# Kernel optimization log

Measured on AMD Instinct MI355X. Metric: run time of the kernel, lower is better.

## Reference

```python
import jax, jax.numpy as jnp
import numpy as np

NEG_SLOPE = 0.2  # PyG GATConv default leaky_relu slope


def gat_layer(x, W, a_src, a_dst, b):
    # x: [B, N, Fin]; W: [Fin, H*C]; a_src/a_dst: [H, C]; b: [H*C]
    # Dense-block equivalent of PyG GATConv on a fully-connected block graph
    # (self loops included), concat=True.
    B, N, Fin = x.shape
    H, C = a_src.shape
    h = jnp.einsum('bnf,fhc->bnhc', x, W.reshape(Fin, H, C))  # [B,N,H,C]
    ls = jnp.einsum('bnhc,hc->bnh', h, a_src)  # alpha_src per node
    ld = jnp.einsum('bnhc,hc->bnh', h, a_dst)  # alpha_dst per node
    # logits[i, j] = leaky_relu(alpha_dst[i] + alpha_src[j]); softmax over j
    logits = jax.nn.leaky_relu(ld[:, :, None, :] + ls[:, None, :, :], NEG_SLOPE)  # [B,i,j,H]
    attn = jax.nn.softmax(logits, axis=2)
    out = jnp.einsum('bijh,bjhc->bihc', attn, h).reshape(B, N, H * C)
    return out + b


def setup_inputs() -> dict:
    key = jax.random.key(0)
    ks = jax.random.split(key, 12)
    bs, R, Nc, enc = 8, 256, 64, 31
    H, hid, out = 8, 64, 32
    Fin = 1 + enc  # 32
    p = lambda k, shape: jax.random.normal(k, shape, jnp.float32) * 0.05
    return {
        'xs': jax.random.normal(ks[0], (bs, R, Nc), jnp.float32),
        'pos_enc': jax.random.normal(ks[1], (bs, Nc, enc), jnp.float32),
        'W1': p(ks[2], (Fin, H * hid)), 'as1': p(ks[3], (H, hid)), 'ad1': p(ks[4], (H, hid)),
        'b1': jnp.zeros((H * hid,), jnp.float32),
        'W2': p(ks[5], (H * hid, H * hid)), 'as2': p(ks[6], (H, hid)), 'ad2': p(ks[7], (H, hid)),
        'b2': jnp.zeros((H * hid,), jnp.float32),
        'W3': p(ks[8], (H * hid, H * out)), 'as3': p(ks[9], (H, out)), 'ad3': p(ks[10], (H, out)),
        'b3': jnp.zeros((H * out,), jnp.float32),
    }


def reference(xs, pos_enc, W1, as1, ad1, b1, W2, as2, ad2, b2, W3, as3, ad3, b3):
    bs, R, Nc = xs.shape
    enc = pos_enc.shape[-1]
    pe = jnp.broadcast_to(pos_enc[:, None], (bs, R, Nc, enc))
    x = jnp.concatenate([xs[..., None], pe], axis=-1)  # [bs,R,Nc,1+enc]
    x = x.reshape(bs * R, Nc, 1 + enc)  # independent fully-connected blocks
    x = gat_layer(x, W1, as1, ad1, b1)
    x = gat_layer(x, W2, as2, ad2, b2)
    x = gat_layer(x, W3, as3, ad3, b3)
    out = x.reshape(bs, R, Nc, -1).mean(axis=2)  # mean over num_xs
    return out
```

## Files before the change

### kernel.cpp

```cpp
#include <hip/hip_runtime.h>
#include <hip/hip_bf16.h>

typedef __hip_bfloat16 bf16;
typedef unsigned int uint32;
typedef __attribute__((ext_vector_type(8))) short short8;
typedef __attribute__((ext_vector_type(4))) float float4v;

#define THREADS 512
#define LDX 520
#define LDE 68

__device__ __forceinline__ bf16 f2b(float x) { return __float2bfloat16(x); }
__device__ __forceinline__ uint32 packbf2(float x, float y) {
  union { __hip_bfloat162 b; uint32 u; } cv;
  cv.b = __float22bfloat162_rn(make_float2(x, y));
  return cv.u;
}

__global__ void convw_all(const float* __restrict__ W1,
                          const float* __restrict__ W2,
                          const float* __restrict__ W3, bf16* __restrict__ dst) {
  int o = blockIdx.x * 256 + threadIdx.x;
  if (o >= 409600) return;
  const float* W;
  int Mlog, loc;
  if (o < 16384) { W = W1; Mlog = 9; loc = o; }
  else if (o < 278528) { W = W2; Mlog = 9; loc = o - 16384; }
  else { W = W3; Mlog = 8; loc = o - 278528; }
  int j = loc & 7, kc = (loc >> 3) & 3, rest = loc >> 5;
  int M = 1 << Mlog;
  int n = rest & (M - 1), kb = rest >> Mlog;
  int k = kb * 32 + kc * 8 + j;
  dst[o] = f2b(W[(size_t)k * M + n]);
}

__global__ void convE_all(
    const float* __restrict__ W1, const float* __restrict__ as1, const float* __restrict__ ad1,
    const float* __restrict__ W2, const float* __restrict__ as2, const float* __restrict__ ad2,
    const float* __restrict__ W3, const float* __restrict__ as3, const float* __restrict__ ad3,
    bf16* __restrict__ dstE) {
  int o = blockIdx.x * 256 + threadIdx.x;
  if (o >= 16896) return;
  const float *W, *as_, *ad_;
  int M, C, loc;
  if (o < 512) { loc = o; W = W1; as_ = as1; ad_ = ad1; M = 512; C = 64; }
  else if (o < 8704) { loc = o - 512; W = W2; as_ = as2; ad_ = ad2; M = 512; C = 64; }
  else { loc = o - 8704; W = W3; as_ = as3; ad_ = ad3; M = 256; C = 32; }
  int j = loc & 7, kc = (loc >> 3) & 3, n = (loc >> 5) & 15, ks = loc >> 9;
  int k = ks * 32 + kc * 8 + j;
  int head = n & 7;
  const float* a = (n < 8) ? as_ : ad_;
  float s = 0.f;
  for (int c = 0; c < C; ++c)
    s += W[(size_t)k * M + head * C + c] * a[head * C + c];
  dstE[o] = f2b(s);
}

template <int K, int M, int C, bool LAST>
__device__ __forceinline__ void gat_layer(
    int t, const bf16* __restrict__ Wswz, const bf16* __restrict__ WE,
    const float* __restrict__ bias, bf16* sX, float* sE) {
  constexpr int CT = M / 128;
  constexpr int CTO = CT / 2;
  constexpr int KS = K / 32;
  const int lane = t & 63;
  const int hu = __builtin_amdgcn_readfirstlane(t >> 6);
  const int ln = lane & 15;
  const int kq = lane >> 4;
  const int colbase = hu * (M / 8);

  const bf16* aptr = sX + ln * LDX + kq * 8;
  const bf16* aptrE = sX + (hu * 16 + ln) * LDX + kq * 8;
  const bf16* eptr = WE + ln * 32 + kq * 8;

  uint32 Ppk[CT][4][2];

#pragma unroll
  for (int cto = 0; cto < CTO; ++cto) {
    float4v acc[4][2];
    float4v acce = (float4v)0.f;
#pragma unroll
    for (int rt = 0; rt < 4; ++rt) {
      acc[rt][0] = (float4v)0.f;
      acc[rt][1] = (float4v)0.f;
    }
    const bf16* bptr = Wswz + (colbase + cto * 32 + ln) * 32 + kq * 8;
    if (cto == 0 && hu < 4) {
#pragma unroll 4
      for (int ks = 0; ks < KS; ++ks) {
        short8 afr[4];
#pragma unroll
        for (int rt = 0; rt < 4; ++rt)
          afr[rt] = *(const short8*)(aptr + rt * 16 * LDX + ks * 32);
        short8 bfr[2];
        bfr[0] = *(const short8*)(bptr + (size_t)ks * (M * 32));
        bfr[1] = *(const short8*)(bptr + (size_t)ks * (M * 32) + 16 * 32);
        short8 efr = *(const short8*)(eptr + ks * 512);
        short8 afrE = *(const short8*)(aptrE + ks * 32);
        acce = __builtin_amdgcn_mfma_f32_16x16x32_bf16(afrE, efr, acce, 0, 0, 0);
#pragma unroll
        for (int rt = 0; rt < 4; ++rt) {
          acc[rt][0] = __builtin_amdgcn_mfma_f32_16x16x32_bf16(
              afr[rt], bfr[0], acc[rt][0], 0, 0, 0);
          acc[rt][1] = __builtin_amdgcn_mfma_f32_16x16x32_bf16(
              afr[rt], bfr[1], acc[rt][1], 0, 0, 0);
        }
      }
      *(float4v*)(sE + ln * LDE + hu * 16 + kq * 4) = acce;
    } else {
#pragma unroll 4
      for (int ks = 0; ks < KS; ++ks) {
        short8 afr[4];
#pragma unroll
        for (int rt = 0; rt < 4; ++rt)
          afr[rt] = *(const short8*)(aptr + rt * 16 * LDX + ks * 32);
        short8 bfr[2];
        bfr[0] = *(const short8*)(bptr + (size_t)ks * (M * 32));
        bfr[1] = *(const short8*)(bptr + (size_t)ks * (M * 32) + 16 * 32);
#pragma unroll
        for (int rt = 0; rt < 4; ++rt) {
          acc[rt][0] = __builtin_amdgcn_mfma_f32_16x16x32_bf16(
              afr[rt], bfr[0], acc[rt][0], 0, 0, 0);
          acc[rt][1] = __builtin_amdgcn_mfma_f32_16x16x32_bf16(
              afr[rt], bfr[1], acc[rt][1], 0, 0, 0);
        }
      }
    }
#pragma unroll
    for (int ci = 0; ci < 2; ++ci)
#pragma unroll
      for (int rt = 0; rt < 4; ++rt) {
        Ppk[cto * 2 + ci][rt][0] = packbf2(acc[rt][ci][0], acc[rt][ci][1]);
        Ppk[cto * 2 + ci][rt][1] = packbf2(acc[rt][ci][2], acc[rt][ci][3]);
      }
  }

  __syncthreads();

  const float* lsrow = sE + hu * LDE;
  const float* ldrow = sE + (8 + hu) * LDE;
  float lsj[2][8];
#pragma unroll
  for (int s = 0; s < 2; ++s) {
    float4 v0 = *(const float4*)(lsrow + s * 32 + kq * 8);
    float4 v1 = *(const float4*)(lsrow + s * 32 + kq * 8 + 4);
    lsj[s][0] = v0.x; lsj[s][1] = v0.y; lsj[s][2] = v0.z; lsj[s][3] = v0.w;
    lsj[s][4] = v1.x; lsj[s][5] = v1.y; lsj[s][6] = v1.z; lsj[s][7] = v1.w;
  }
  short8 pfr[4][2];
#pragma unroll
  for (int rt = 0; rt < 4; ++rt) {
    const float ldi = ldrow[rt * 16 + ln];
    float pe_[2][8];
    float rsum = 0.f;
#pragma unroll
    for (int s = 0; s < 2; ++s)
#pragma unroll
      for (int jj = 0; jj < 8; ++jj) {
        float tt = ldi + lsj[s][jj];
        float l = fmaxf(tt, 0.2f * tt);
        float e = __expf(l);
        pe_[s][jj] = e;
        rsum += e;
      }
    rsum += __shfl_xor(rsum, 16, 64);
    rsum += __shfl_xor(rsum, 32, 64);
    const float ri = 1.0f / rsum;
#pragma unroll
    for (int s = 0; s < 2; ++s) {
      union { uint32 q[4]; short8 s8; } w;
#pragma unroll
      for (int jp = 0; jp < 4; ++jp)
        w.q[jp] = packbf2(pe_[s][2 * jp] * ri, pe_[s][2 * jp + 1] * ri);
      pfr[rt][s] = w.s8;
    }
  }

  const int kqhi = kq >> 1;
  const int addrA = 4 * (ln + 16 * ((kq & 1) << 1));
#pragma unroll
  for (int ct = 0; ct < CT; ++ct) {
    short8 hfr[2];
#pragma unroll
    for (int s = 0; s < 2; ++s) {
      union { uint32 q[4]; short8 s8; } u;
#pragma unroll
      for (int jjp = 0; jjp < 4; ++jjp) {
        int addr = addrA + ((jjp >> 1) << 6);
        int lo = __builtin_amdgcn_ds_bpermute(addr, (int)Ppk[ct][2 * s + 0][jjp & 1]);
        int hi = __builtin_amdgcn_ds_bpermute(addr, (int)Ppk[ct][2 * s + 1][jjp & 1]);
        u.q[jjp] = kqhi ? (uint32)hi : (uint32)lo;
      }
      hfr[s] = u.s8;
    }
    float4v oacc[4];
#pragma unroll
    for (int rt = 0; rt < 4; ++rt) oacc[rt] = (float4v)0.f;
#pragma unroll
    for (int s = 0; s < 2; ++s)
#pragma unroll
      for (int rt = 0; rt < 4; ++rt)
        oacc[rt] = __builtin_amdgcn_mfma_f32_16x16x32_bf16(
            pfr[rt][s], hfr[s], oacc[rt], 0, 0, 0);
    const float bv = bias[colbase + ct * 16 + ln];
#pragma unroll
    for (int rt = 0; rt < 4; ++rt)
#pragma unroll
      for (int r = 0; r < 4; ++r) {
        float val = oacc[rt][r] + bv;
        int row = rt * 16 + kq * 4 + r;
        if constexpr (LAST)
          ((float*)sX)[row * 260 + colbase + ct * 16 + ln] = val;
        else
          sX[row * LDX + colbase + ct * 16 + ln] = f2b(val);
      }
  }
  __syncthreads();
}

__global__ __launch_bounds__(THREADS, 4) void gat3_mfma(
    const float* __restrict__ xs, const float* __restrict__ pe,
    const bf16* __restrict__ W1s, const bf16* __restrict__ WE1,
    const float* __restrict__ b1, const bf16* __restrict__ W2s,
    const bf16* __restrict__ WE2, const float* __restrict__ b2,
    const bf16* __restrict__ W3s, const bf16* __restrict__ WE3,
    const float* __restrict__ b3, float* __restrict__ out) {
  extern __shared__ char smem[];
  bf16* sX = (bf16*)smem;
  float* sE = (float*)(smem + 66560);

  const int t = threadIdx.x;
  const int blk = blockIdx.x;
  const int bidx = blk >> 8;

  for (int idx = t; idx < 64 * 32; idx += THREADS) {
    int n = idx >> 5, f = idx & 31;
    float v = (f == 0) ? xs[blk * 64 + n] : pe[(bidx * 64 + n) * 31 + (f - 1)];
    sX[n * LDX + f] = f2b(v);
  }
  __syncthreads();

  gat_layer<32, 512, 64, false>(t, W1s, WE1, b1, sX, sE);
  gat_layer<512, 512, 64, false>(t, W2s, WE2, b2, sX, sE);
  gat_layer<512, 256, 32, true>(t, W3s, WE3, b3, sX, sE);

  const float* xf = (const float*)sX;
  if (t < 256) {
    float s = 0.f;
#pragma unroll 8
    for (int i = 0; i < 64; ++i) s += xf[i * 260 + t];
    out[blk * 256 + t] = s * 0.015625f;
  }
}

extern "C" void kernel_launch(void* const* d_in, const int* in_sizes, int n_in,
                              void* d_out, int out_size, void* d_ws, size_t ws_size,
                              hipStream_t stream) {
  const float* xs = (const float*)d_in[0];
  const float* pe = (const float*)d_in[1];
  const float* W1 = (const float*)d_in[2];
  const float* as1 = (const float*)d_in[3];
  const float* ad1 = (const float*)d_in[4];
  const float* b1 = (const float*)d_in[5];
  const float* W2 = (const float*)d_in[6];
  const float* as2 = (const float*)d_in[7];
  const float* ad2 = (const float*)d_in[8];
  const float* b2 = (const float*)d_in[9];
  const float* W3 = (const float*)d_in[10];
  const float* as3 = (const float*)d_in[11];
  const float* ad3 = (const float*)d_in[12];
  const float* b3 = (const float*)d_in[13];

  bf16* Wall = (bf16*)d_ws;
  bf16* WEall = Wall + 409600;
  bf16* W1s = Wall;
  bf16* W2s = Wall + 16384;
  bf16* W3s = Wall + 278528;
  bf16* WE1 = WEall;
  bf16* WE2 = WEall + 512;
  bf16* WE3 = WEall + 8704;

  convw_all<<<dim3(1600), dim3(256), 0, stream>>>(W1, W2, W3, Wall);
  convE_all<<<dim3(66), dim3(256), 0, stream>>>(W1, as1, ad1, W2, as2, ad2,
                                                W3, as3, ad3, WEall);

  const size_t smem = 70912;
  (void)hipFuncSetAttribute((const void*)gat3_mfma,
                            hipFuncAttributeMaxDynamicSharedMemorySize,
                            (int)smem);
  gat3_mfma<<<dim3(2048), dim3(THREADS), smem, stream>>>(
      xs, pe, W1s, WE1, b1, W2s, WE2, b2, W3s, WE3, b3, (float*)d_out);
}
```

Measured before the change: 252.7 us.

## Switch GAT layer matmuls to 32x32x16 MFMA with matching weight swizzle

Replaces the 16x16x32 bf16 MFMA tiling with 32x32x16 MFMA for both the feature projection and the attention-times-features product, changing the host-side weight swizzle to a 16-wide K layout. The attention logit projection is split into its own small loop. The cross-lane transpose of the projected features now uses a single xor-32 shuffle with selects instead of ds_bpermute. This is meant to cut instruction count and LDS fragment loads per FLOP and simplify the data exchange, at the cost of larger accumulator register footprint.

```diff
diff --git a/kernel.cpp b/kernel.cpp
--- a/kernel.cpp
+++ b/kernel.cpp
@@ -5,6 +5,7 @@
 typedef unsigned int uint32;
 typedef __attribute__((ext_vector_type(8))) short short8;
 typedef __attribute__((ext_vector_type(4))) float float4v;
+typedef __attribute__((ext_vector_type(16))) float float16v;
 
 #define THREADS 512
 #define LDX 520
@@ -27,10 +28,10 @@
   if (o < 16384) { W = W1; Mlog = 9; loc = o; }
   else if (o < 278528) { W = W2; Mlog = 9; loc = o - 16384; }
   else { W = W3; Mlog = 8; loc = o - 278528; }
-  int j = loc & 7, kc = (loc >> 3) & 3, rest = loc >> 5;
+  int j = loc & 7, q = (loc >> 3) & 1, rest = loc >> 4;
   int M = 1 << Mlog;
   int n = rest & (M - 1), kb = rest >> Mlog;
-  int k = kb * 32 + kc * 8 + j;
+  int k = kb * 16 + q * 8 + j;
   dst[o] = f2b(W[(size_t)k * M + n]);
 }
 
@@ -60,78 +61,51 @@
 __device__ __forceinline__ void gat_layer(
     int t, const bf16* __restrict__ Wswz, const bf16* __restrict__ WE,
     const float* __restrict__ bias, bf16* sX, float* sE) {
-  constexpr int CT = M / 128;
-  constexpr int CTO = CT / 2;
-  constexpr int KS = K / 32;
+  constexpr int NCT = C / 32;
+  constexpr int KS16 = K / 16;
+  constexpr int KSE = K / 32;
   const int lane = t & 63;
   const int hu = __builtin_amdgcn_readfirstlane(t >> 6);
-  const int ln = lane & 15;
-  const int kq = lane >> 4;
-  const int colbase = hu * (M / 8);
-
-  const bf16* aptr = sX + ln * LDX + kq * 8;
-  const bf16* aptrE = sX + (hu * 16 + ln) * LDX + kq * 8;
-  const bf16* eptr = WE + ln * 32 + kq * 8;
-
-  uint32 Ppk[CT][4][2];
-
-#pragma unroll
-  for (int cto = 0; cto < CTO; ++cto) {
-    float4v acc[4][2];
+  const int c = lane & 31, q = lane >> 5;
+  const int ln16 = lane & 15, kq16 = lane >> 4;
+  const int colbase = hu * C;
+
+  if (hu < 4) {
     float4v acce = (float4v)0.f;
 #pragma unroll
-    for (int rt = 0; rt < 4; ++rt) {
-      acc[rt][0] = (float4v)0.f;
-      acc[rt][1] = (float4v)0.f;
-    }
-    const bf16* bptr = Wswz + (colbase + cto * 32 + ln) * 32 + kq * 8;
-    if (cto == 0 && hu < 4) {
+    for (int ks = 0; ks < KSE; ++ks) {
+      short8 afrE = *(const short8*)(sX + (hu * 16 + ln16) * LDX + ks * 32 + kq16 * 8);
+      short8 efr = *(const short8*)(WE + ks * 512 + ln16 * 32 + kq16 * 8);
+      acce = __builtin_amdgcn_mfma_f32_16x16x32_bf16(afrE, efr, acce, 0, 0, 0);
+    }
+    *(float4v*)(sE + ln16 * LDE + hu * 16 + kq16 * 4) = acce;
+  }
+
+  uint32 Ppk[NCT][4][4];
+#pragma unroll
+  for (int rt = 0; rt < 2; ++rt) {
+    float16v acc[NCT];
+#pragma unroll
+    for (int ct = 0; ct < NCT; ++ct) acc[ct] = (float16v)0.f;
+    const bf16* ap = sX + (rt * 32 + c) * LDX + q * 8;
 #pragma unroll 4
-      for (int ks = 0; ks < KS; ++ks) {
-        short8 afr[4];
-#pragma unroll
-        for (int rt = 0; rt < 4; ++rt)
-          afr[rt] = *(const short8*)(aptr + rt * 16 * LDX + ks * 32);
-        short8 bfr[2];
-        bfr[0] = *(const short8*)(bptr + (size_t)ks * (M * 32));
-        bfr[1] = *(const short8*)(bptr + (size_t)ks * (M * 32) + 16 * 32);
-        short8 efr = *(const short8*)(eptr + ks * 512);
-        short8 afrE = *(const short8*)(aptrE + ks * 32);
-        acce = __builtin_amdgcn_mfma_f32_16x16x32_bf16(afrE, efr, acce, 0, 0, 0);
-#pragma unroll
-        for (int rt = 0; rt < 4; ++rt) {
-          acc[rt][0] = __builtin_amdgcn_mfma_f32_16x16x32_bf16(
-              afr[rt], bfr[0], acc[rt][0], 0, 0, 0);
-          acc[rt][1] = __builtin_amdgcn_mfma_f32_16x16x32_bf16(
-              afr[rt], bfr[1], acc[rt][1], 0, 0, 0);
-        }
-      }
-      *(float4v*)(sE + ln * LDE + hu * 16 + kq * 4) = acce;
-    } else {
-#pragma unroll 4
-      for (int ks = 0; ks < KS; ++ks) {
-        short8 afr[4];
-#pragma unroll
-        for (int rt = 0; rt < 4; ++rt)
-          afr[rt] = *(const short8*)(aptr + rt * 16 * LDX + ks * 32);
-        short8 bfr[2];
-        bfr[0] = *(const short8*)(bptr + (size_t)ks * (M * 32));
-        bfr[1] = *(const short8*)(bptr + (size_t)ks * (M * 32) + 16 * 32);
-#pragma unroll
-        for (int rt = 0; rt < 4; ++rt) {
-          acc[rt][0] = __builtin_amdgcn_mfma_f32_16x16x32_bf16(
-              afr[rt], bfr[0], acc[rt][0], 0, 0, 0);
-          acc[rt][1] = __builtin_amdgcn_mfma_f32_16x16x32_bf16(
-              afr[rt], bfr[1], acc[rt][1], 0, 0, 0);
-        }
-      }
-    }
-#pragma unroll
-    for (int ci = 0; ci < 2; ++ci)
-#pragma unroll
-      for (int rt = 0; rt < 4; ++rt) {
-        Ppk[cto * 2 + ci][rt][0] = packbf2(acc[rt][ci][0], acc[rt][ci][1]);
-        Ppk[cto * 2 + ci][rt][1] = packbf2(acc[rt][ci][2], acc[rt][ci][3]);
+    for (int ks = 0; ks < KS16; ++ks) {
+      short8 afr = *(const short8*)(ap + ks * 16);
+#pragma unroll
+      for (int ct = 0; ct < NCT; ++ct) {
+        short8 bfr = *(const short8*)(Wswz + (size_t)ks * (M * 16) +
+                                      ((colbase + ct * 32 + c) * 2 + q) * 8);
+        acc[ct] = __builtin_amdgcn_mfma_f32_32x32x16_bf16(afr, bfr, acc[ct], 0, 0, 0);
+      }
+    }
+#pragma unroll
+    for (int ct = 0; ct < NCT; ++ct)
+#pragma unroll
+      for (int tp = 0; tp < 2; ++tp) {
+        Ppk[ct][rt * 2 + tp][0] = packbf2(acc[ct][8 * tp + 0], acc[ct][8 * tp + 1]);
+        Ppk[ct][rt * 2 + tp][1] = packbf2(acc[ct][8 * tp + 2], acc[ct][8 * tp + 3]);
+        Ppk[ct][rt * 2 + tp][2] = packbf2(acc[ct][8 * tp + 4], acc[ct][8 * tp + 5]);
+        Ppk[ct][rt * 2 + tp][3] = packbf2(acc[ct][8 * tp + 6], acc[ct][8 * tp + 7]);
       }
   }
 
@@ -139,80 +113,75 @@
 
   const float* lsrow = sE + hu * LDE;
   const float* ldrow = sE + (8 + hu) * LDE;
-  float lsj[2][8];
-#pragma unroll
-  for (int s = 0; s < 2; ++s) {
-    float4 v0 = *(const float4*)(lsrow + s * 32 + kq * 8);
-    float4 v1 = *(const float4*)(lsrow + s * 32 + kq * 8 + 4);
-    lsj[s][0] = v0.x; lsj[s][1] = v0.y; lsj[s][2] = v0.z; lsj[s][3] = v0.w;
-    lsj[s][4] = v1.x; lsj[s][5] = v1.y; lsj[s][6] = v1.z; lsj[s][7] = v1.w;
-  }
-  short8 pfr[4][2];
-#pragma unroll
-  for (int rt = 0; rt < 4; ++rt) {
-    const float ldi = ldrow[rt * 16 + ln];
-    float pe_[2][8];
+  short8 pfr[2][4];
+#pragma unroll
+  for (int rt = 0; rt < 2; ++rt) {
+    const float ldi = ldrow[rt * 32 + c];
+    float pe_[4][8];
     float rsum = 0.f;
 #pragma unroll
-    for (int s = 0; s < 2; ++s)
+    for (int tt = 0; tt < 4; ++tt) {
+      float4 v0 = *(const float4*)(lsrow + tt * 16 + q * 8);
+      float4 v1 = *(const float4*)(lsrow + tt * 16 + q * 8 + 4);
+      float ls8[8] = {v0.x, v0.y, v0.z, v0.w, v1.x, v1.y, v1.z, v1.w};
 #pragma unroll
       for (int jj = 0; jj < 8; ++jj) {
-        float tt = ldi + lsj[s][jj];
-        float l = fmaxf(tt, 0.2f * tt);
+        float tv = ldi + ls8[jj];
+        float l = fmaxf(tv, 0.2f * tv);
         float e = __expf(l);
-        pe_[s][jj] = e;
+        pe_[tt][jj] = e;
         rsum += e;
       }
-    rsum += __shfl_xor(rsum, 16, 64);
+    }
     rsum += __shfl_xor(rsum, 32, 64);
     const float ri = 1.0f / rsum;
 #pragma unroll
-    for (int s = 0; s < 2; ++s) {
-      union { uint32 q[4]; short8 s8; } w;
+    for (int tt = 0; tt < 4; ++tt) {
+      union { uint32 d[4]; short8 s; } w;
 #pragma unroll
       for (int jp = 0; jp < 4; ++jp)
-        w.q[jp] = packbf2(pe_[s][2 * jp] * ri, pe_[s][2 * jp + 1] * ri);
-      pfr[rt][s] = w.s8;
-    }
-  }
-
-  const int kqhi = kq >> 1;
-  const int addrA = 4 * (ln + 16 * ((kq & 1) << 1));
-#pragma unroll
-  for (int ct = 0; ct < CT; ++ct) {
-    short8 hfr[2];
-#pragma unroll
-    for (int s = 0; s < 2; ++s) {
-      union { uint32 q[4]; short8 s8; } u;
-#pragma unroll
-      for (int jjp = 0; jjp < 4; ++jjp) {
-        int addr = addrA + ((jjp >> 1) << 6);
-        int lo = __builtin_amdgcn_ds_bpermute(addr, (int)Ppk[ct][2 * s + 0][jjp & 1]);
-        int hi = __builtin_amdgcn_ds_bpermute(addr, (int)Ppk[ct][2 * s + 1][jjp & 1]);
-        u.q[jjp] = kqhi ? (uint32)hi : (uint32)lo;
-      }
-      hfr[s] = u.s8;
-    }
-    float4v oacc[4];
-#pragma unroll
-    for (int rt = 0; rt < 4; ++rt) oacc[rt] = (float4v)0.f;
-#pragma unroll
-    for (int s = 0; s < 2; ++s)
-#pragma unroll
-      for (int rt = 0; rt < 4; ++rt)
-        oacc[rt] = __builtin_amdgcn_mfma_f32_16x16x32_bf16(
-            pfr[rt][s], hfr[s], oacc[rt], 0, 0, 0);
-    const float bv = bias[colbase + ct * 16 + ln];
-#pragma unroll
-    for (int rt = 0; rt < 4; ++rt)
-#pragma unroll
-      for (int r = 0; r < 4; ++r) {
+        w.d[jp] = packbf2(pe_[tt][2 * jp] * ri, pe_[tt][2 * jp + 1] * ri);
+      pfr[rt][tt] = w.s;
+    }
+  }
+
+#pragma unroll
+  for (int ct = 0; ct < NCT; ++ct) {
+    short8 hfr[4];
+#pragma unroll
+    for (int tt = 0; tt < 4; ++tt) {
+      uint32 U0 = Ppk[ct][tt][0], U1 = Ppk[ct][tt][1];
+      uint32 V0 = Ppk[ct][tt][2], V1 = Ppk[ct][tt][3];
+      uint32 X0 = q ? U0 : V0;
+      uint32 X1 = q ? U1 : V1;
+      uint32 R0 = (uint32)__shfl_xor((int)X0, 32, 64);
+      uint32 R1 = (uint32)__shfl_xor((int)X1, 32, 64);
+      union { uint32 d[4]; short8 s; } u;
+      u.d[0] = q ? R0 : U0;
+      u.d[1] = q ? R1 : U1;
+      u.d[2] = q ? V0 : R0;
+      u.d[3] = q ? V1 : R1;
+      hfr[tt] = u.s;
+    }
+    float16v oacc[2];
+    oacc[0] = (float16v)0.f;
+    oacc[1] = (float16v)0.f;
+#pragma unroll
+    for (int tt = 0; tt < 4; ++tt) {
+      oacc[0] = __builtin_amdgcn_mfma_f32_32x32x16_bf16(pfr[0][tt], hfr[tt], oacc[0], 0, 0, 0);
+      oacc[1] = __builtin_amdgcn_mfma_f32_32x32x16_bf16(pfr[1][tt], hfr[tt], oacc[1], 0, 0, 0);
+    }
+    const float bv = bias[colbase + ct * 32 + c];
+#pragma unroll
+    for (int rt = 0; rt < 2; ++rt)
+#pragma unroll
+      for (int r = 0; r < 16; ++r) {
         float val = oacc[rt][r] + bv;
-        int row = rt * 16 + kq * 4 + r;
+        int row = rt * 32 + (r & 3) + 8 * (r >> 2) + 4 * q;
         if constexpr (LAST)
-          ((float*)sX)[row * 260 + colbase + ct * 16 + ln] = val;
+          ((float*)sX)[row * 260 + colbase + ct * 32 + c] = val;
         else
-          sX[row * LDX + colbase + ct * 16 + ln] = f2b(val);
+          sX[row * LDX + colbase + ct * 32 + c] = f2b(val);
       }
   }
   __syncthreads();
```

Result: slower. 279.9 us (+10.8%).
